# Performance work log

Measured on AMD Instinct MI355X. Metric: run time of the kernel, lower is better.

## Reference

```python
import jax, jax.numpy as jnp
import numpy as np

B, CIN, COUT, COFF = 1, 16, 32, 16
D, H, W = 32, 128, 160
K = 3
EPS = 1e-5  # torch BatchNorm default


def conv2d(x, w):
    return jax.lax.conv_general_dilated(x, w, (1, 1), [(1, 1), (1, 1)],
                                        dimension_numbers=('NCHW', 'OIHW', 'NCHW'))


def conv3d(x, w):
    return jax.lax.conv_general_dilated(x, w, (1, 1, 1), [(1, 1), (1, 1), (1, 1)],
                                        dimension_numbers=('NCDHW', 'OIDHW', 'NCDHW'))


def bn(x, gamma, beta, axes):
    # training-mode batch norm (batch statistics), matching torch BN in train mode
    m = jnp.mean(x, axis=axes, keepdims=True)
    v = jnp.var(x, axis=axes, keepdims=True)
    sh = [1] * x.ndim
    sh[1] = -1
    return (x - m) * jax.lax.rsqrt(v + EPS) * gamma.reshape(sh) + beta.reshape(sh)


def bilinear_gather(x, py, px):
    # x: [B,C,H,W]; py,px: [B,K2,H,W] float sample coords -> [B,C,K2,H,W]
    Bq, C, Hh, Ww = x.shape
    y0 = jnp.floor(py)
    x0 = jnp.floor(px)
    wy1 = py - y0
    wx1 = px - x0

    def g(yi, xi):
        yic = jnp.clip(yi, 0, Hh - 1).astype(jnp.int32)
        xic = jnp.clip(xi, 0, Ww - 1).astype(jnp.int32)
        mask = ((yi >= 0) & (yi <= Hh - 1) & (xi >= 0) & (xi <= Ww - 1)).astype(x.dtype)
        v = jax.vmap(lambda xb, yb, xc: xb[:, yb, xc])(x, yic, xic)  # [B,C,K2,H,W]
        return v * mask[:, None]

    return (g(y0, x0) * ((1.0 - wy1) * (1.0 - wx1))[:, None]
            + g(y0, x0 + 1.0) * ((1.0 - wy1) * wx1)[:, None]
            + g(y0 + 1.0, x0) * (wy1 * (1.0 - wx1))[:, None]
            + g(y0 + 1.0, x0 + 1.0) * (wy1 * wx1)[:, None])


def gd_slice(xs, ds, w_off, w_reg, g1, b1):
    # DeformableConv2dBnReLU on one depth slice: xs [B,CIN,H,W], ds [B,COFF,H,W]
    offset = jnp.clip(conv2d(ds, w_off), -1.0, 1.0)     # [B, 2*K*K, H, W]
    Bq = offset.shape[0]
    off = offset.reshape(Bq, K * K, 2, H, W)            # torchvision layout: (dy, dx) per tap
    ii = jnp.repeat(jnp.arange(K), K).astype(xs.dtype)  # kernel row index per tap
    jj = jnp.tile(jnp.arange(K), K).astype(xs.dtype)    # kernel col index per tap
    # base sampling grid (stride=1, pad=1, dilation=1) plus learned offsets
    py = (jnp.arange(H, dtype=xs.dtype)[None, :, None] - 1.0 + ii[:, None, None])[None] + off[:, :, 0]
    px = (jnp.arange(W, dtype=xs.dtype)[None, None, :] - 1.0 + jj[:, None, None])[None] + off[:, :, 1]
    sampled = bilinear_gather(xs, py, px)               # [B,CIN,K2,H,W]
    out = jnp.einsum('bckhw,ock->bohw', sampled, w_reg.reshape(COUT, CIN, K * K))
    return jax.nn.relu(bn(out, g1, b1, (0, 2, 3)))      # per-slice BN2d stats, as in the torch loop


def setup_inputs() -> dict:
    key = jax.random.key(0)
    ks = jax.random.split(key, 6)
    r = lambda k, sh, s=1.0: jax.random.normal(k, sh, dtype=jnp.float32) * s
    return {
        'x': r(ks[0], (B, CIN, D, H, W)),
        'f': r(ks[1], (B, COFF, D, H, W)),
        'w_off': r(ks[2], (2 * K * K, COFF, 3, 3), 0.05),
        'w_reg': r(ks[3], (COUT, CIN, K, K), 0.1),
        'g1': jnp.ones((COUT,), jnp.float32),
        'b1': jnp.zeros((COUT,), jnp.float32),
        'w2': r(ks[4], (COUT, COUT, K, K, K), 0.05),
        'g2': jnp.ones((COUT,), jnp.float32),
        'b2': jnp.zeros((COUT,), jnp.float32),
        'wd': r(ks[5], (COUT, CIN, K, K, K), 0.05),
        'gd': jnp.ones((COUT,), jnp.float32),
        'bd': jnp.zeros((COUT,), jnp.float32),
    }


def reference(x, f, w_off, w_reg, g1, b1, w2, g2, b2, wd, gd, bd):
    # GDConv3D: per-depth-slice deformable conv + BN2d + ReLU, vmapped over D
    out = jax.vmap(gd_slice, in_axes=(2, 2, None, None, None, None), out_axes=2)(
        x, f, w_off, w_reg, g1, b1)                      # [B,COUT,D,H,W]
    out = bn(conv3d(out, w2), g2, b2, (0, 2, 3, 4))
    identity = bn(conv3d(x, wd), gd, bd, (0, 2, 3, 4))   # downsample (CIN != COUT)
    return jax.nn.relu(out + identity)
```

## Files before the change

kernel.cpp:

```cpp
#include <hip/hip_runtime.h>

using u16 = unsigned short;

constexpr int CIN = 16, COUT = 32, COFF = 16;
constexpr int D = 32, H = 128, W = 160;
constexpr int HW = H * W;
constexpr int DHW = D * HW;
constexpr int NOUT = COUT * DHW;
constexpr float EPS = 1e-5f;

constexpr size_t WF_OFF = 16384;
constexpr size_t A1CH_OFF = 262144;
constexpr size_t XCH16_OFF = 42205184;
constexpr size_t FRAG2P_W2 = 84148224;
constexpr size_t FRAG2P_WD = 84203520;
constexpr size_t NEED_2PASS = 84258816;
constexpr size_t STA_OFF = 63176704;
constexpr size_t STB_OFF = 147062784;
constexpr size_t FRAGS_W2 = 230948864;
constexpr size_t FRAGS_WD = 231004160;
constexpr size_t NEED_STORE = 231059456;
constexpr int WOFF_O = 0, WREG_O = 2592, W2_O = 7200, WD_O = 34848;
constexpr int G1_O = 48672, B1_O = 48704, G2_O = 48736, B2_O = 48768, GD_O = 48800, BD_O = 48832;
constexpr int FLAG_SLOT = 3000;

typedef short bf16x8 __attribute__((ext_vector_type(8)));
typedef float f32x4 __attribute__((ext_vector_type(4)));

static __device__ __forceinline__ float bf2f(u16 h) {
  unsigned u = ((unsigned)h) << 16;
  float f;
  __builtin_memcpy(&f, &u, 4);
  return f;
}
static __device__ __forceinline__ u16 f2bf(float f) {
  unsigned u;
  __builtin_memcpy(&u, &f, 4);
  u += 0x7fffu + ((u >> 16) & 1u);
  return (u16)(u >> 16);
}
static __device__ __forceinline__ float ldin(const void* p, int i, int bf) {
  float r;
  if (bf) r = bf2f(((const u16*)p)[i]);
  else r = ((const float*)p)[i];
  return r;
}

__global__ __launch_bounds__(256) void zero_kernel(float* __restrict__ S) {
  S[blockIdx.x * 256 + threadIdx.x] = 0.f;
}

__global__ __launch_bounds__(256) void sniff_kernel(const u16* __restrict__ x,
                                                    int* __restrict__ flag) {
  __shared__ int sh[256];
  int cnt = 0;
  for (int i = threadIdx.x; i < 4096; i += 256) {
    int e = (x[i] >> 7) & 0xff;
    cnt += (e >= 96 && e <= 144) ? 1 : 0;
  }
  sh[threadIdx.x] = cnt;
  __syncthreads();
  for (int s = 128; s > 0; s >>= 1) {
    if (threadIdx.x < (unsigned)s) sh[threadIdx.x] += sh[threadIdx.x + s];
    __syncthreads();
  }
  if (threadIdx.x == 0) flag[0] = (sh[0] > 3072) ? 1 : 0;
}

__global__ __launch_bounds__(256) void cvt_kernel(const void* __restrict__ in,
                                                  float* __restrict__ out, int n,
                                                  const int* __restrict__ flagp) {
  int bf = flagp[0];
  int i = blockIdx.x * 256 + threadIdx.x;
  if (i < n) out[i] = ldin(in, i, bf);
}

__global__ __launch_bounds__(256) void pack_frag_kernel(const float* __restrict__ src,
                                                        u16* __restrict__ dst, int nci) {
  int t = blockIdx.x * 256 + threadIdx.x;
  if (t >= 27648) return;
  int j = t & 7;
  int l = (t >> 3) & 63;
  int cotile = (t >> 9) & 1;
  int tap = t >> 10;
  int co = cotile * 16 + (l & 15);
  int k = (l >> 4) * 8 + j;
  float v = (k < nci) ? src[(co * nci + k) * 27 + tap] : 0.f;
  dst[t] = f2bf(v);
}

__global__ __launch_bounds__(256) void chpose_kernel(const void* __restrict__ src,
                                                     u16* __restrict__ dst,
                                                     const int* __restrict__ flagp) {
  const int bf = flagp[0];
  __shared__ u16 lt[16][258];
  const int base = blockIdx.x * 256;
  const int t = threadIdx.x;
#pragma unroll
  for (int ci = 0; ci < 16; ci++) lt[ci][t] = f2bf(ldin(src, ci * DHW + base + t, bf));
  __syncthreads();
  const size_t pb = (size_t)(base + t) * 16;
  uint4 u0, u1;
  u0.x = (unsigned)lt[0][t] | ((unsigned)lt[1][t] << 16);
  u0.y = (unsigned)lt[2][t] | ((unsigned)lt[3][t] << 16);
  u0.z = (unsigned)lt[4][t] | ((unsigned)lt[5][t] << 16);
  u0.w = (unsigned)lt[6][t] | ((unsigned)lt[7][t] << 16);
  u1.x = (unsigned)lt[8][t] | ((unsigned)lt[9][t] << 16);
  u1.y = (unsigned)lt[10][t] | ((unsigned)lt[11][t] << 16);
  u1.z = (unsigned)lt[12][t] | ((unsigned)lt[13][t] << 16);
  u1.w = (unsigned)lt[14][t] | ((unsigned)lt[15][t] << 16);
  *(uint4*)(dst + pb) = u0;
  *(uint4*)(dst + pb + 8) = u1;
}

__global__ __launch_bounds__(256) void deform_chm_kernel(const void* __restrict__ x,
                                                         const void* __restrict__ f,
                                                         const float* __restrict__ w_off_f,
                                                         const float* __restrict__ w_reg_f,
                                                         u16* __restrict__ a1ch,
                                                         const int* __restrict__ flagp,
                                                         float* __restrict__ S) {
  const int bf = flagp[0];
  const int hw = blockIdx.x;
  const int bid = (hw & 7) * 320 + (hw >> 3);
  const int d = bid / 80;
  const int p = (bid % 80) * 256 + threadIdx.x;
  const int y = p / W;
  const int xx = p % W;
  const int dbase = d * HW;

  float doff[18];
#pragma unroll
  for (int t = 0; t < 18; t++) doff[t] = 0.f;
  for (int ci = 0; ci < COFF; ci++) {
    const int fbase = ci * DHW + dbase;
#pragma unroll
    for (int ki = 0; ki < 3; ki++) {
      int yy = y - 1 + ki;
      bool yok = (unsigned)yy < (unsigned)H;
#pragma unroll
      for (int kj = 0; kj < 3; kj++) {
        int xj = xx - 1 + kj;
        float v = (yok && (unsigned)xj < (unsigned)W) ? ldin(f, fbase + yy * W + xj, bf) : 0.f;
        int widx = ci * 9 + ki * 3 + kj;
#pragma unroll
        for (int t = 0; t < 18; t++) doff[t] += v * w_off_f[t * 144 + widx];
      }
    }
  }

  float acc[COUT];
#pragma unroll
  for (int co = 0; co < COUT; co++) acc[co] = 0.f;

#pragma unroll
  for (int t = 0; t < 9; t++) {
    float dy = fminf(fmaxf(doff[2 * t], -1.f), 1.f);
    float dx = fminf(fmaxf(doff[2 * t + 1], -1.f), 1.f);
    float py = (float)(y - 1 + t / 3) + dy;
    float px = (float)(xx - 1 + t % 3) + dx;
    float y0f = floorf(py), x0f = floorf(px);
    float wy1 = py - y0f, wx1 = px - x0f;
    int y0 = (int)y0f, x0i = (int)x0f;
    int y1 = y0 + 1, x1 = x0i + 1;
    bool y0v = (unsigned)y0 < (unsigned)H, y1v = (unsigned)y1 < (unsigned)H;
    bool x0v = (unsigned)x0i < (unsigned)W, x1v = (unsigned)x1 < (unsigned)W;
    float c00 = (y0v && x0v) ? (1.f - wy1) * (1.f - wx1) : 0.f;
    float c01 = (y0v && x1v) ? (1.f - wy1) * wx1 : 0.f;
    float c10 = (y1v && x0v) ? wy1 * (1.f - wx1) : 0.f;
    float c11 = (y1v && x1v) ? wy1 * wx1 : 0.f;
    int y0c = min(max(y0, 0), H - 1) * W, y1c = min(max(y1, 0), H - 1) * W;
    int x0c = min(max(x0i, 0), W - 1), x1c = min(max(x1, 0), W - 1);

    for (int ci = 0; ci < CIN; ci++) {
      const int xbase = ci * DHW + dbase;
      float s = c00 * ldin(x, xbase + y0c + x0c, bf) + c01 * ldin(x, xbase + y0c + x1c, bf) +
                c10 * ldin(x, xbase + y1c + x0c, bf) + c11 * ldin(x, xbase + y1c + x1c, bf);
#pragma unroll
      for (int co = 0; co < COUT; co++) acc[co] += s * w_reg_f[co * 144 + ci * 9 + t];
    }
  }

  u16 hh[COUT];
#pragma unroll
  for (int co = 0; co < COUT; co++) hh[co] = f2bf(acc[co]);
  const size_t pb = ((size_t)dbase + p) * 32;
#pragma unroll
  for (int k = 0; k < 4; k++) {
    uint4 u;
    u.x = (unsigned)hh[8 * k + 0] | ((unsigned)hh[8 * k + 1] << 16);
    u.y = (unsigned)hh[8 * k + 2] | ((unsigned)hh[8 * k + 3] << 16);
    u.z = (unsigned)hh[8 * k + 4] | ((unsigned)hh[8 * k + 5] << 16);
    u.w = (unsigned)hh[8 * k + 6] | ((unsigned)hh[8 * k + 7] << 16);
    *(uint4*)(a1ch + pb + 8 * k) = u;
  }

  const int l = threadIdx.x & 63;
  const int wv = threadIdx.x >> 6;
  __shared__ float ls[128], lq[128];
#pragma unroll
  for (int co = 0; co < COUT; co++) {
    float v = bf2f(hh[co]);
    float s = v, qq = v * v;
    s += __shfl_xor(s, 1);  qq += __shfl_xor(qq, 1);
    s += __shfl_xor(s, 2);  qq += __shfl_xor(qq, 2);
    s += __shfl_xor(s, 4);  qq += __shfl_xor(qq, 4);
    s += __shfl_xor(s, 8);  qq += __shfl_xor(qq, 8);
    s += __shfl_xor(s, 16); qq += __shfl_xor(qq, 16);
    s += __shfl_xor(s, 32); qq += __shfl_xor(qq, 32);
    if (l == 0) { ls[wv * 32 + co] = s; lq[wv * 32 + co] = qq; }
  }
  __syncthreads();
  if (threadIdx.x < 32) {
    int c = threadIdx.x;
    float s = ls[c] + ls[32 + c] + ls[64 + c] + ls[96 + c];
    float qq = lq[c] + lq[32 + c] + lq[64 + c] + lq[96 + c];
    atomicAdd(&S[c * D + d], s);
    atomicAdd(&S[1024 + c * D + d], qq);
  }
}

__global__ __launch_bounds__(256) void bn1_scale_kernel(float* __restrict__ S,
                                                        const float* __restrict__ g1f,
                                                        const float* __restrict__ b1f) {
  int cd = blockIdx.x * 256 + threadIdx.x;
  if (cd >= 1024) return;
  int c = cd / D;
  float mean = S[cd] / (float)HW;
  float var = S[1024 + cd] / (float)HW - mean * mean;
  float sc = g1f[c] * rsqrtf(var + EPS);
  S[cd] = sc;
  S[1024 + cd] = b1f[c] - mean * sc;
}

__global__ __launch_bounds__(256) void bn1_apply_ch_kernel(u16* __restrict__ a1ch,
                                                           const float* __restrict__ S) {
  __shared__ float sc[32], of[32];
  const int b = blockIdx.x;
  const int d = b / (HW / 256);
  if (threadIdx.x < 32) {
    sc[threadIdx.x] = S[threadIdx.x * D + d];
    of[threadIdx.x] = S[1024 + threadIdx.x * D + d];
  }
  __syncthreads();
  const size_t pb = ((size_t)b * 256 + threadIdx.x) * 32;
#pragma unroll
  for (int k = 0; k < 4; k++) {
    uint4 u = *(const uint4*)(a1ch + pb + 8 * k);
    unsigned w[4] = {u.x, u.y, u.z, u.w};
    unsigned ov[4];
#pragma unroll
    for (int m = 0; m < 4; m++) {
      int c0 = k * 8 + m * 2;
      float lo = bf2f((u16)(w[m] & 0xffffu));
      float hi = bf2f((u16)(w[m] >> 16));
      lo = fmaxf(lo * sc[c0] + of[c0], 0.f);
      hi = fmaxf(hi * sc[c0 + 1] + of[c0 + 1], 0.f);
      ov[m] = (unsigned)f2bf(lo) | ((unsigned)f2bf(hi) << 16);
    }
    uint4 o;
    o.x = ov[0]; o.y = ov[1]; o.z = ov[2]; o.w = ov[3];
    *(uint4*)(a1ch + pb + 8 * k) = o;
  }
}

typedef u16 u16x8 __attribute__((ext_vector_type(8)));
static __device__ __forceinline__ void conv_core_lds(const bf16x8* __restrict__ a1v,
                                                     const bf16x8* __restrict__ xv16,
                                                     const bf16x8* __restrict__ w2s,
                                                     const bf16x8* __restrict__ wdv,
                                                     int d, int y, int xn, int q, int l,
                                                     f32x4& A0, f32x4& A1, f32x4& B0, f32x4& B1) {
  const bf16x8 zero = {0, 0, 0, 0, 0, 0, 0, 0};
  const bool qlo = (q < 2);
#pragma unroll
  for (int kd = 0; kd < 3; kd++) {
    int dd = d - 1 + kd;
    if ((unsigned)dd >= (unsigned)D) continue;
#pragma unroll
    for (int ky = 0; ky < 3; ky++) {
      int yy = y - 1 + ky;
      if ((unsigned)yy >= (unsigned)H) continue;
      const int rowb = dd * HW + yy * W;
#pragma unroll
      for (int kx = 0; kx < 3; kx++) {
        int xx = xn - 1 + kx;
        bool ok = (unsigned)xx < (unsigned)W;
        int xc = min(max(xx, 0), W - 1);
        int pi = rowb + xc;
        bf16x8 bm = a1v[pi * 4 + q];
        bf16x8 bx = qlo ? xv16[pi * 2 + q] : zero;
        if (!ok) { bm = zero; bx = zero; }
        const int tb = (kd * 9 + ky * 3 + kx) * 2;
        bf16x8 am0 = w2s[(tb + 0) * 64 + l];
        bf16x8 am1 = w2s[(tb + 1) * 64 + l];
        bf16x8 ad0 = qlo ? wdv[(tb + 0) * 64 + l] : zero;
        bf16x8 ad1 = qlo ? wdv[(tb + 1) * 64 + l] : zero;
        A0 = __builtin_amdgcn_mfma_f32_16x16x32_bf16(am0, bm, A0, 0, 0, 0);
        A1 = __builtin_amdgcn_mfma_f32_16x16x32_bf16(am1, bm, A1, 0, 0, 0);
        B0 = __builtin_amdgcn_mfma_f32_16x16x32_bf16(ad0, bx, B0, 0, 0, 0);
        B1 = __builtin_amdgcn_mfma_f32_16x16x32_bf16(ad1, bx, B1, 0, 0, 0);
      }
    }
  }
}

#define STATS_RED(ACC, BASE)                                                          \
  {                                                                                   \
    _Pragma("unroll") for (int r = 0; r < 4; r++) {                                   \
      float v = ACC[r];                                                               \
      float s = v, qq = v * v;                                                        \
      s += __shfl_xor(s, 1); qq += __shfl_xor(qq, 1);                                 \
      s += __shfl_xor(s, 2); qq += __shfl_xor(qq, 2);                                 \
      s += __shfl_xor(s, 4); qq += __shfl_xor(qq, 4);                                 \
      s += __shfl_xor(s, 8); qq += __shfl_xor(qq, 8);                                 \
      if (n == 0) {                                                                   \
        int ci = (BASE) + q * 4 + r;                                                  \
        ls[wv * 64 + ci] = s;                                                         \
        lq[wv * 64 + ci] = qq;                                                        \
      }                                                                               \
    }                                                                                 \
  }

__global__ __launch_bounds__(1024) void conv_mfma_store_kernel(const u16* __restrict__ a1ch,
                                                               const u16* __restrict__ xch16,
                                                               const u16* __restrict__ w2f,
                                                               const u16* __restrict__ wdf,
                                                               float* __restrict__ A,
                                                               float* __restrict__ Bb,
                                                               float* __restrict__ S) {
  __shared__ u16 w2s[27648];
  __shared__ float ls[16 * 64], lq[16 * 64];
  {
    const uint4* src = (const uint4*)w2f;
    uint4* dst = (uint4*)w2s;
    for (int i = threadIdx.x; i < 3456; i += 1024) dst[i] = src[i];
  }
  __syncthreads();

  const int hw = blockIdx.x;
  const int bid = (hw & 7) * 320 + (hw >> 3);
  const int t = threadIdx.x;
  const int l = t & 63, wv = t >> 6;
  const int n = l & 15, q = l >> 4;
  const int P = bid * 256 + wv * 16;
  const int d = P / HW;
  const int rp = P % HW;
  const int y = rp / W, xc0 = rp % W;

  f32x4 A0 = {0.f, 0.f, 0.f, 0.f}, A1 = {0.f, 0.f, 0.f, 0.f};
  f32x4 B0 = {0.f, 0.f, 0.f, 0.f}, B1 = {0.f, 0.f, 0.f, 0.f};
  conv_core_lds((const bf16x8*)a1ch, (const bf16x8*)xch16, (const bf16x8*)w2s,
                (const bf16x8*)wdf, d, y, xc0 + n, q, l, A0, A1, B0, B1);

#pragma unroll
  for (int r = 0; r < 4; r++) {
    int co = q * 4 + r;
    A[co * DHW + P + n] = A0[r];
    A[(co + 16) * DHW + P + n] = A1[r];
    Bb[co * DHW + P + n] = B0[r];
    Bb[(co + 16) * DHW + P + n] = B1[r];
  }

  STATS_RED(A0, 0)
  STATS_RED(A1, 16)
  STATS_RED(B0, 32)
  STATS_RED(B1, 48)
  __syncthreads();
  if (t < 64) {
    float s = 0.f, qq = 0.f;
    for (int w = 0; w < 16; w++) { s += ls[w * 64 + t]; qq += lq[w * 64 + t]; }
    if (t < 32) {
      atomicAdd(&S[2048 + t], s);
      atomicAdd(&S[2080 + t], qq);
    } else {
      atomicAdd(&S[2112 + t - 32], s);
      atomicAdd(&S[2144 + t - 32], qq);
    }
  }
}

__global__ __launch_bounds__(1024) void conv_mfma_stats_kernel(const u16* __restrict__ a1ch,
                                                               const u16* __restrict__ xch16,
                                                               const u16* __restrict__ w2f,
                                                               const u16* __restrict__ wdf,
                                                               float* __restrict__ S) {
  __shared__ u16 w2s[27648];
  __shared__ float ls[16 * 64], lq[16 * 64];
  {
    const uint4* src = (const uint4*)w2f;
    uint4* dst = (uint4*)w2s;
    for (int i = threadIdx.x; i < 3456; i += 1024) dst[i] = src[i];
  }
  __syncthreads();

  const int hw = blockIdx.x;
  const int bid = (hw & 7) * 320 + (hw >> 3);
  const int t = threadIdx.x;
  const int l = t & 63, wv = t >> 6;
  const int n = l & 15, q = l >> 4;
  const int P = bid * 256 + wv * 16;
  const int d = P / HW;
  const int rp = P % HW;
  const int y = rp / W, xc0 = rp % W;

  f32x4 A0 = {0.f, 0.f, 0.f, 0.f}, A1 = {0.f, 0.f, 0.f, 0.f};
  f32x4 B0 = {0.f, 0.f, 0.f, 0.f}, B1 = {0.f, 0.f, 0.f, 0.f};
  conv_core_lds((const bf16x8*)a1ch, (const bf16x8*)xch16, (const bf16x8*)w2s,
                (const bf16x8*)wdf, d, y, xc0 + n, q, l, A0, A1, B0, B1);

  STATS_RED(A0, 0)
  STATS_RED(A1, 16)
  STATS_RED(B0, 32)
  STATS_RED(B1, 48)
  __syncthreads();
  if (t < 64) {
    float s = 0.f, qq = 0.f;
    for (int w = 0; w < 16; w++) { s += ls[w * 64 + t]; qq += lq[w * 64 + t]; }
    if (t < 32) {
      atomicAdd(&S[2048 + t], s);
      atomicAdd(&S[2080 + t], qq);
    } else {
      atomicAdd(&S[2112 + t - 32], s);
      atomicAdd(&S[2144 + t - 32], qq);
    }
  }
}

__global__ void bn3_final_kernel(float* __restrict__ S, const float* __restrict__ g2f,
                                 const float* __restrict__ b2f, const float* __restrict__ gdf,
                                 const float* __restrict__ bdf) {
  int t = threadIdx.x;
  if (t < 32) {
    float mean = S[2048 + t] / (float)DHW;
    float var = S[2080 + t] / (float)DHW - mean * mean;
    float sc = g2f[t] * rsqrtf(var + EPS);
    S[2176 + t] = sc;
    S[2208 + t] = b2f[t] - mean * sc;
  } else {
    int c = t - 32;
    float mean = S[2112 + c] / (float)DHW;
    float var = S[2144 + c] / (float)DHW - mean * mean;
    float sc = gdf[c] * rsqrtf(var + EPS);
    S[2240 + c] = sc;
    S[2272 + c] = bdf[c] - mean * sc;
  }
}

__global__ __launch_bounds__(256) void combine32_kernel(const float* __restrict__ A,
                                                        const float* __restrict__ Bb,
                                                        const float* __restrict__ S,
                                                        const int* __restrict__ flagp,
                                                        void* __restrict__ out) {
  int i = (blockIdx.x * 256 + threadIdx.x) * 4;
  int co = i / DHW;
  float s2 = S[2176 + co], o2 = S[2208 + co];
  float sd = S[2240 + co], od = S[2272 + co];
  float4 va = *(const float4*)(A + i);
  float4 vb = *(const float4*)(Bb + i);
  float r0 = fmaxf(va.x * s2 + o2 + vb.x * sd + od, 0.f);
  float r1 = fmaxf(va.y * s2 + o2 + vb.y * sd + od, 0.f);
  float r2 = fmaxf(va.z * s2 + o2 + vb.z * sd + od, 0.f);
  float r3 = fmaxf(va.w * s2 + o2 + vb.w * sd + od, 0.f);
  int bf = flagp[0];
  if (bf) {
    ushort4 st;
    st.x = f2bf(r0); st.y = f2bf(r1); st.z = f2bf(r2); st.w = f2bf(r3);
    *(ushort4*)((u16*)out + i) = st;
  } else {
    float4 st;
    st.x = r0; st.y = r1; st.z = r2; st.w = r3;
    *(float4*)((float*)out + i) = st;
  }
}

__global__ __launch_bounds__(256) void conv_mfma_final_kernel(const u16* __restrict__ a1ch,
                                                              const u16* __restrict__ xch16,
                                                              const u16* __restrict__ w2f,
                                                              const u16* __restrict__ wdf,
                                                              const float* __restrict__ S,
                                                              const int* __restrict__ flagp,
                                                              void* __restrict__ out) {
  __shared__ u16 w2s[27648];
  {
    const uint4* src = (const uint4*)w2f;
    uint4* dst = (uint4*)w2s;
    for (int i = threadIdx.x; i < 3456; i += 256) dst[i] = src[i];
  }
  __syncthreads();

  const int hw = blockIdx.x;
  const int bid = (hw & 7) * 1280 + (hw >> 3);
  const int t = threadIdx.x;
  const int l = t & 63, wv = t >> 6;
  const int n = l & 15, q = l >> 4;
  const int P = bid * 64 + wv * 16;
  const int d = P / HW;
  const int rp = P % HW;
  const int y = rp / W, xc0 = rp % W;

  f32x4 A0 = {0.f, 0.f, 0.f, 0.f}, A1 = {0.f, 0.f, 0.f, 0.f};
  f32x4 B0 = {0.f, 0.f, 0.f, 0.f}, B1 = {0.f, 0.f, 0.f, 0.f};
  conv_core_lds((const bf16x8*)a1ch, (const bf16x8*)xch16, (const bf16x8*)w2s,
                (const bf16x8*)wdf, d, y, xc0 + n, q, l, A0, A1, B0, B1);

  const int bf = flagp[0];
#pragma unroll
  for (int r = 0; r < 4; r++) {
    int co = q * 4 + r;
    {
      float s2 = S[2176 + co], o2 = S[2208 + co];
      float sd = S[2240 + co], od = S[2272 + co];
      float v = fmaxf(A0[r] * s2 + o2 + B0[r] * sd + od, 0.f);
      int ai = co * DHW + P + n;
      if (bf) ((u16*)out)[ai] = f2bf(v);
      else ((float*)out)[ai] = v;
    }
    {
      int c2 = co + 16;
      float s2 = S[2176 + c2], o2 = S[2208 + c2];
      float sd = S[2240 + c2], od = S[2272 + c2];
      float v = fmaxf(A1[r] * s2 + o2 + B1[r] * sd + od, 0.f);
      int ai = c2 * DHW + P + n;
      if (bf) ((u16*)out)[ai] = f2bf(v);
      else ((float*)out)[ai] = v;
    }
  }
}

extern "C" void kernel_launch(void* const* d_in, const int* in_sizes, int n_in,
                              void* d_out, int out_size, void* d_ws, size_t ws_size,
                              hipStream_t stream) {
  const void* x = d_in[0];
  const void* f = d_in[1];

  char* ws = (char*)d_ws;
  float* S = (float*)ws;
  int* flag = (int*)ws + FLAG_SLOT;
  float* WF = (float*)(ws + WF_OFF);
  u16* a1ch = (u16*)(ws + A1CH_OFF);
  u16* xch16 = (u16*)(ws + XCH16_OFF);

  zero_kernel<<<16, 256, 0, stream>>>(S);
  sniff_kernel<<<1, 256, 0, stream>>>((const u16*)x, flag);

  const int cvt_n[10] = {2592, 4608, 27648, 13824, 32, 32, 32, 32, 32, 32};
  const int cvt_off[10] = {WOFF_O, WREG_O, W2_O, WD_O, G1_O, B1_O, G2_O, B2_O, GD_O, BD_O};
  const int src_idx[10] = {2, 3, 6, 9, 4, 5, 7, 8, 10, 11};
  for (int k = 0; k < 10; k++) {
    cvt_kernel<<<(cvt_n[k] + 255) / 256, 256, 0, stream>>>(d_in[src_idx[k]], WF + cvt_off[k],
                                                           cvt_n[k], flag);
  }

  const int store = (ws_size >= NEED_STORE) ? 1 : 0;
  u16* w2frag = (u16*)(ws + (store ? FRAGS_W2 : FRAG2P_W2));
  u16* wdfrag = (u16*)(ws + (store ? FRAGS_WD : FRAG2P_WD));

  pack_frag_kernel<<<108, 256, 0, stream>>>(WF + W2_O, w2frag, 32);
  pack_frag_kernel<<<108, 256, 0, stream>>>(WF + WD_O, wdfrag, 16);
  chpose_kernel<<<DHW / 256, 256, 0, stream>>>(x, xch16, flag);

  deform_chm_kernel<<<2560, 256, 0, stream>>>(x, f, WF + WOFF_O, WF + WREG_O, a1ch, flag, S);
  bn1_scale_kernel<<<4, 256, 0, stream>>>(S, WF + G1_O, WF + B1_O);
  bn1_apply_ch_kernel<<<DHW / 256, 256, 0, stream>>>(a1ch, S);

  if (store) {
    float* A = (float*)(ws + STA_OFF);
    float* Bb = (float*)(ws + STB_OFF);
    conv_mfma_store_kernel<<<2560, 1024, 0, stream>>>(a1ch, xch16, w2frag, wdfrag, A, Bb, S);
    bn3_final_kernel<<<1, 64, 0, stream>>>(S, WF + G2_O, WF + B2_O, WF + GD_O, WF + BD_O);
    combine32_kernel<<<NOUT / 1024, 256, 0, stream>>>(A, Bb, S, flag, d_out);
  } else {
    conv_mfma_stats_kernel<<<2560, 1024, 0, stream>>>(a1ch, xch16, w2frag, wdfrag, S);
    bn3_final_kernel<<<1, 64, 0, stream>>>(S, WF + G2_O, WF + B2_O, WF + GD_O, WF + BD_O);
    conv_mfma_final_kernel<<<10240, 256, 0, stream>>>(a1ch, xch16, w2frag, wdfrag, S, flag,
                                                      d_out);
  }
}
```

Measured before the change: 813.5 us.

## Process two pixel groups per wave in conv MFMA and transpose deform weights

```diff
diff --git a/kernel.cpp b/kernel.cpp
--- a/kernel.cpp
+++ b/kernel.cpp
@@ -22,6 +22,7 @@
 constexpr size_t NEED_STORE = 231059456;
 constexpr int WOFF_O = 0, WREG_O = 2592, W2_O = 7200, WD_O = 34848;
 constexpr int G1_O = 48672, B1_O = 48704, G2_O = 48736, B2_O = 48768, GD_O = 48800, BD_O = 48832;
+constexpr int WOFFT_O = 49152, WREGT_O = 52224;
 constexpr int FLAG_SLOT = 3000;
 
 typedef short bf16x8 __attribute__((ext_vector_type(8)));
@@ -73,6 +74,22 @@
   int bf = flagp[0];
   int i = blockIdx.x * 256 + threadIdx.x;
   if (i < n) out[i] = ldin(in, i, bf);
+}
+
+__global__ __launch_bounds__(256) void woff_t_kernel(const float* __restrict__ src,
+                                                     float* __restrict__ dst) {
+  int t = blockIdx.x * 256 + threadIdx.x;
+  if (t >= 2592) return;
+  int ch = t / 144, widx = t % 144;
+  dst[widx * 18 + ch] = src[t];
+}
+
+__global__ __launch_bounds__(256) void wreg_t_kernel(const float* __restrict__ src,
+                                                     float* __restrict__ dst) {
+  int t = blockIdx.x * 256 + threadIdx.x;
+  if (t >= 4608) return;
+  int co = t / 144, k = t % 144;
+  dst[k * 32 + co] = src[t];
 }
 
 __global__ __launch_bounds__(256) void pack_frag_kernel(const float* __restrict__ src,
@@ -115,8 +132,8 @@
 
 __global__ __launch_bounds__(256) void deform_chm_kernel(const void* __restrict__ x,
                                                          const void* __restrict__ f,
-                                                         const float* __restrict__ w_off_f,
-                                                         const float* __restrict__ w_reg_f,
+                                                         const float* __restrict__ w_off_t,
+                                                         const float* __restrict__ w_reg_t,
                                                          u16* __restrict__ a1ch,
                                                          const int* __restrict__ flagp,
                                                          float* __restrict__ S) {
@@ -144,7 +161,7 @@
         float v = (yok && (unsigned)xj < (unsigned)W) ? ldin(f, fbase + yy * W + xj, bf) : 0.f;
         int widx = ci * 9 + ki * 3 + kj;
 #pragma unroll
-        for (int t = 0; t < 18; t++) doff[t] += v * w_off_f[t * 144 + widx];
+        for (int t = 0; t < 18; t++) doff[t] += v * w_off_t[widx * 18 + t];
       }
     }
   }
@@ -176,8 +193,9 @@
       const int xbase = ci * DHW + dbase;
       float s = c00 * ldin(x, xbase + y0c + x0c, bf) + c01 * ldin(x, xbase + y0c + x1c, bf) +
                 c10 * ldin(x, xbase + y1c + x0c, bf) + c11 * ldin(x, xbase + y1c + x1c, bf);
-#pragma unroll
-      for (int co = 0; co < COUT; co++) acc[co] += s * w_reg_f[co * 144 + ci * 9 + t];
+      const float* wp = w_reg_t + (ci * 9 + t) * 32;
+#pragma unroll
+      for (int co = 0; co < COUT; co++) acc[co] += s * wp[co];
     }
   }
 
@@ -265,6 +283,7 @@
 }
 
 typedef u16 u16x8 __attribute__((ext_vector_type(8)));
+
 static __device__ __forceinline__ void conv_core_lds(const bf16x8* __restrict__ a1v,
                                                      const bf16x8* __restrict__ xv16,
                                                      const bf16x8* __restrict__ w2s,
@@ -322,6 +341,23 @@
     }                                                                                 \
   }
 
+#define STATS_RED2(Aa, Ab, BASE)                                                      \
+  {                                                                                   \
+    _Pragma("unroll") for (int r = 0; r < 4; r++) {                                   \
+      float v0 = Aa[r], v1 = Ab[r];                                                   \
+      float s = v0 + v1, qq = v0 * v0 + v1 * v1;                                      \
+      s += __shfl_xor(s, 1); qq += __shfl_xor(qq, 1);                                 \
+      s += __shfl_xor(s, 2); qq += __shfl_xor(qq, 2);                                 \
+      s += __shfl_xor(s, 4); qq += __shfl_xor(qq, 4);                                 \
+      s += __shfl_xor(s, 8); qq += __shfl_xor(qq, 8);                                 \
+      if (n == 0) {                                                                   \
+        int ci = (BASE) + q * 4 + r;                                                  \
+        ls[wv * 64 + ci] = s;                                                         \
+        lq[wv * 64 + ci] = qq;                                                        \
+      }                                                                               \
+    }                                                                                 \
+  }
+
 __global__ __launch_bounds__(1024) void conv_mfma_store_kernel(const u16* __restrict__ a1ch,
                                                                const u16* __restrict__ xch16,
                                                                const u16* __restrict__ w2f,
@@ -339,33 +375,95 @@
   __syncthreads();
 
   const int hw = blockIdx.x;
-  const int bid = (hw & 7) * 320 + (hw >> 3);
+  const int bid = (hw & 7) * 160 + (hw >> 3);
   const int t = threadIdx.x;
   const int l = t & 63, wv = t >> 6;
   const int n = l & 15, q = l >> 4;
-  const int P = bid * 256 + wv * 16;
-  const int d = P / HW;
-  const int rp = P % HW;
-  const int y = rp / W, xc0 = rp % W;
-
-  f32x4 A0 = {0.f, 0.f, 0.f, 0.f}, A1 = {0.f, 0.f, 0.f, 0.f};
-  f32x4 B0 = {0.f, 0.f, 0.f, 0.f}, B1 = {0.f, 0.f, 0.f, 0.f};
-  conv_core_lds((const bf16x8*)a1ch, (const bf16x8*)xch16, (const bf16x8*)w2s,
-                (const bf16x8*)wdf, d, y, xc0 + n, q, l, A0, A1, B0, B1);
-
-#pragma unroll
-  for (int r = 0; r < 4; r++) {
-    int co = q * 4 + r;
-    A[co * DHW + P + n] = A0[r];
-    A[(co + 16) * DHW + P + n] = A1[r];
-    Bb[co * DHW + P + n] = B0[r];
-    Bb[(co + 16) * DHW + P + n] = B1[r];
-  }
-
-  STATS_RED(A0, 0)
-  STATS_RED(A1, 16)
-  STATS_RED(B0, 32)
-  STATS_RED(B1, 48)
+  const int P0 = bid * 512 + wv * 32;
+  const int d = P0 / HW;
+  const int rp0 = P0 % HW;
+  const int y0 = rp0 / W, x0 = rp0 % W;
+  const int rp1 = (P0 + 16) % HW;
+  const int y1g = rp1 / W, x1g = rp1 % W;
+
+  const bf16x8 zero = {0, 0, 0, 0, 0, 0, 0, 0};
+  const bool qlo = (q < 2);
+  const bf16x8* a1v = (const bf16x8*)a1ch;
+  const bf16x8* xv16 = (const bf16x8*)xch16;
+  const bf16x8* w2v = (const bf16x8*)w2s;
+  const bf16x8* wdv = (const bf16x8*)wdf;
+
+  f32x4 aA0[2], aA1[2], aB0[2], aB1[2];
+#pragma unroll
+  for (int g = 0; g < 2; g++) {
+    aA0[g] = (f32x4){0.f, 0.f, 0.f, 0.f};
+    aA1[g] = (f32x4){0.f, 0.f, 0.f, 0.f};
+    aB0[g] = (f32x4){0.f, 0.f, 0.f, 0.f};
+    aB1[g] = (f32x4){0.f, 0.f, 0.f, 0.f};
+  }
+
+#pragma unroll
+  for (int kd = 0; kd < 3; kd++) {
+    int dd = d - 1 + kd;
+    if ((unsigned)dd >= (unsigned)D) continue;
+#pragma unroll
+    for (int ky = 0; ky < 3; ky++) {
+      int yy0 = y0 - 1 + ky, yy1 = y1g - 1 + ky;
+      bool yok0 = (unsigned)yy0 < (unsigned)H, yok1 = (unsigned)yy1 < (unsigned)H;
+      int rb0 = dd * HW + min(max(yy0, 0), H - 1) * W;
+      int rb1 = dd * HW + min(max(yy1, 0), H - 1) * W;
+#pragma unroll
+      for (int kx = 0; kx < 3; kx++) {
+        const int tb = (kd * 9 + ky * 3 + kx) * 2;
+        bf16x8 am0 = w2v[(tb + 0) * 64 + l];
+        bf16x8 am1 = w2v[(tb + 1) * 64 + l];
+        bf16x8 ad0 = qlo ? wdv[(tb + 0) * 64 + l] : zero;
+        bf16x8 ad1 = qlo ? wdv[(tb + 1) * 64 + l] : zero;
+        {
+          int xx = x0 + n - 1 + kx;
+          bool ok = yok0 && (unsigned)xx < (unsigned)W;
+          int pi = rb0 + min(max(xx, 0), W - 1);
+          bf16x8 bm = a1v[pi * 4 + q];
+          bf16x8 bx = qlo ? xv16[pi * 2 + q] : zero;
+          if (!ok) { bm = zero; bx = zero; }
+          aA0[0] = __builtin_amdgcn_mfma_f32_16x16x32_bf16(am0, bm, aA0[0], 0, 0, 0);
+          aA1[0] = __builtin_amdgcn_mfma_f32_16x16x32_bf16(am1, bm, aA1[0], 0, 0, 0);
+          aB0[0] = __builtin_amdgcn_mfma_f32_16x16x32_bf16(ad0, bx, aB0[0], 0, 0, 0);
+          aB1[0] = __builtin_amdgcn_mfma_f32_16x16x32_bf16(ad1, bx, aB1[0], 0, 0, 0);
+        }
+        {
+          int xx = x1g + n - 1 + kx;
+          bool ok = yok1 && (unsigned)xx < (unsigned)W;
+          int pi = rb1 + min(max(xx, 0), W - 1);
+          bf16x8 bm = a1v[pi * 4 + q];
+          bf16x8 bx = qlo ? xv16[pi * 2 + q] : zero;
+          if (!ok) { bm = zero; bx = zero; }
+          aA0[1] = __builtin_amdgcn_mfma_f32_16x16x32_bf16(am0, bm, aA0[1], 0, 0, 0);
+          aA1[1] = __builtin_amdgcn_mfma_f32_16x16x32_bf16(am1, bm, aA1[1], 0, 0, 0);
+          aB0[1] = __builtin_amdgcn_mfma_f32_16x16x32_bf16(ad0, bx, aB0[1], 0, 0, 0);
+          aB1[1] = __builtin_amdgcn_mfma_f32_16x16x32_bf16(ad1, bx, aB1[1], 0, 0, 0);
+        }
+      }
+    }
+  }
+
+#pragma unroll
+  for (int g = 0; g < 2; g++) {
+    const int Pg = P0 + 16 * g;
+#pragma unroll
+    for (int r = 0; r < 4; r++) {
+      int co = q * 4 + r;
+      A[co * DHW + Pg + n] = aA0[g][r];
+      A[(co + 16) * DHW + Pg + n] = aA1[g][r];
+      Bb[co * DHW + Pg + n] = aB0[g][r];
+      Bb[(co + 16) * DHW + Pg + n] = aB1[g][r];
+    }
+  }
+
+  STATS_RED2(aA0[0], aA0[1], 0)
+  STATS_RED2(aA1[0], aA1[1], 16)
+  STATS_RED2(aB0[0], aB0[1], 32)
+  STATS_RED2(aB1[0], aB1[1], 48)
   __syncthreads();
   if (t < 64) {
     float s = 0.f, qq = 0.f;
@@ -556,18 +654,20 @@
   u16* w2frag = (u16*)(ws + (store ? FRAGS_W2 : FRAG2P_W2));
   u16* wdfrag = (u16*)(ws + (store ? FRAGS_WD : FRAG2P_WD));
 
+  woff_t_kernel<<<11, 256, 0, stream>>>(WF + WOFF_O, WF + WOFFT_O);
+  wreg_t_kernel<<<18, 256, 0, stream>>>(WF + WREG_O, WF + WREGT_O);
   pack_frag_kernel<<<108, 256, 0, stream>>>(WF + W2_O, w2frag, 32);
   pack_frag_kernel<<<108, 256, 0, stream>>>(WF + WD_O, wdfrag, 16);
   chpose_kernel<<<DHW / 256, 256, 0, stream>>>(x, xch16, flag);
 
-  deform_chm_kernel<<<2560, 256, 0, stream>>>(x, f, WF + WOFF_O, WF + WREG_O, a1ch, flag, S);
+  deform_chm_kernel<<<2560, 256, 0, stream>>>(x, f, WF + WOFFT_O, WF + WREGT_O, a1ch, flag, S);
   bn1_scale_kernel<<<4, 256, 0, stream>>>(S, WF + G1_O, WF + B1_O);
   bn1_apply_ch_kernel<<<DHW / 256, 256, 0, stream>>>(a1ch, S);
 
   if (store) {
     float* A = (float*)(ws + STA_OFF);
     float* Bb = (float*)(ws + STB_OFF);
-    conv_mfma_store_kernel<<<2560, 1024, 0, stream>>>(a1ch, xch16, w2frag, wdfrag, A, Bb, S);
+    conv_mfma_store_kernel<<<1280, 1024, 0, stream>>>(a1ch, xch16, w2frag, wdfrag, A, Bb, S);
     bn3_final_kernel<<<1, 64, 0, stream>>>(S, WF + G2_O, WF + B2_O, WF + GD_O, WF + BD_O);
     combine32_kernel<<<NOUT / 1024, 256, 0, stream>>>(A, Bb, S, flag, d_out);
   } else {
```

After: 731.1 us. 10.1% less time.
